# Performance work log

Measured on AMD Instinct MI355X. Metric: run time of the kernel, lower is better.

The kernel has to match this reference:

```python
import jax, jax.numpy as jnp
import numpy as np

N_CLASSES = 19


def setup_inputs() -> dict:
    key = jax.random.key(0)
    k1, k2 = jax.random.split(key)
    embedding = jax.random.normal(k1, (4, 32, 128, 128), dtype=jnp.float32)
    label = jax.random.randint(k2, (4, 512, 512), 0, N_CLASSES, dtype=jnp.int64)
    return {"embedding": embedding, "label": label}


def _discriminative_loss(embedding, label, n_classes=N_CLASSES):
    N, H, W = label.shape
    C = embedding.shape[1]
    # bilinear upsample embedding to label resolution (F.upsample mode='bilinear')
    emb = jax.image.resize(embedding, (N, C, H, W), method="bilinear")
    HW = H * W
    emb = emb.reshape(N, C, HW).transpose(0, 2, 1)          # (N, HW, C)
    lab = label.reshape(N, HW)                               # (N, HW)

    onehot = jax.nn.one_hot(lab, n_classes, dtype=emb.dtype)  # (N, HW, K)
    count = onehot.sum(1)                                    # (N, K)
    mask = (count > 0).astype(emb.dtype)                     # (N, K)

    # per-class embedding sum and (biased, /(count+1)) mean
    cls_sum = jnp.einsum("npc,npk->nkc", emb, onehot)       # (N, K, C)
    cls_mean = cls_sum / (count[:, :, None] + 1.0)           # (N, K, C)

    # intra-class: per-pixel squared distance to own-class mean, mean over C
    mean_pp = jnp.take_along_axis(cls_mean, lab[:, :, None], axis=1)  # (N, HW, C)
    d2 = jnp.mean((emb - mean_pp) ** 2, axis=-1)             # (N, HW)
    intra_per_cls = jnp.einsum("np,npk->nk", d2, onehot) / (count + 1.0)  # (N, K)
    n_fg = mask[:, 1:].sum(1)                                # (N,)
    l2_intra = (intra_per_cls[:, 1:] * mask[:, 1:]).sum(1) / n_fg  # (N,)

    # inter-class: pairwise mean squared distance between class means
    diff = cls_mean[:, :, None, :] - cls_mean[:, None, :, :]  # (N, K, K, C)
    inter = jnp.mean(diff ** 2, axis=-1)                     # (N, K, K)
    inter = inter * mask[:, None, :] * mask[:, :, None]
    l2_inter = inter[:, 1:, 1:].reshape(N, -1).sum(1) / (n_fg * n_fg)  # (N,)

    return l2_intra - l2_inter


def reference(embedding, label):
    return _discriminative_loss(embedding, label)
```

## Files before the change

kernel.cpp:

```cpp
#include <hip/hip_runtime.h>

#define NIMG 4
#define NCLS 19
#define CCH  32
#define LH   128
#define LW   128
#define HH   512
#define WW   512
#define HWQ  (LH*LW)
#define HWP  (HH*WW)

#define TR 8
#define TC 16
#define NTX (LW/TC)
#define NTY (LH/TR)
#define NTILE (NTY*NTX)
#define TCELLS (TR*TC)
#define HALO_R (TR*4+4)
#define HALO_C (TC*4+4)

#define QB 64

__device__ __forceinline__ void taps(int v, int lim, int& i0, int& i1, float& f) {
    int r = v & 3;
    int b = (v >> 2) + ((r < 2) ? -1 : 0);
    f = 0.125f + 0.25f * (float)((r + 2) & 3);
    i0 = b < 0 ? 0 : b;
    i1 = (b + 1 > lim) ? lim : (b + 1);
}

__global__ __launch_bounds__(256) void k_field(const float* __restrict__ E,
        const int* __restrict__ lab, float* __restrict__ P_sum, float* __restrict__ P_cnt) {
    int tile = blockIdx.x, n = blockIdx.y;
    int ty = tile >> 3, tx = tile & 7;
    int Y0 = ty * TR, X0 = tx * TC;
    __shared__ float A[TCELLS * NCLS];
    __shared__ float red[8 * NCLS * CCH];
    int tid = threadIdx.x;
    for (int i = tid; i < TCELLS * NCLS; i += 256) A[i] = 0.f;
    __syncthreads();

    const int* ln = lab + (size_t)n * HWP;
    int h_lo = Y0 * 4 - 2, w_lo = X0 * 4 - 2;
    for (int i = tid; i < HALO_R * HALO_C; i += 256) {
        int hr = i / HALO_C, wc = i - hr * HALO_C;
        int h = h_lo + hr, w = w_lo + wc;
        if (h < 0 || h >= HH || w < 0 || w >= WW) continue;
        int L = ln[h * WW + w];
        int y0, y1, x0, x1; float fy, fx;
        taps(h, LH - 1, y0, y1, fy);
        taps(w, LW - 1, x0, x1, fx);
        int yy[2] = {y0, y1}; float wy[2] = {1.f - fy, fy};
        int xx[2] = {x0, x1}; float wx[2] = {1.f - fx, fx};
#pragma unroll
        for (int a = 0; a < 2; a++) {
#pragma unroll
            for (int b = 0; b < 2; b++) {
                int ry = yy[a] - Y0, rx = xx[b] - X0;
                if (ry >= 0 && ry < TR && rx >= 0 && rx < TC)
                    atomicAdd(&A[(ry * TC + rx) * NCLS + L], wy[a] * wx[b]);
            }
        }
    }
    __syncthreads();

    int g = tid >> 5, c = tid & 31;
    const float* Ec = E + ((size_t)n * CCH + c) * HWQ;
    float acc[NCLS];
#pragma unroll
    for (int k = 0; k < NCLS; k++) acc[k] = 0.f;
#pragma unroll
    for (int j = 0; j < TCELLS / 8; j++) {
        int cell = g * (TCELLS / 8) + j;
        int cy = cell >> 4, cx = cell & 15;
        float e = Ec[(Y0 + cy) * LW + (X0 + cx)];
        const float* Ar = &A[cell * NCLS];
#pragma unroll
        for (int k = 0; k < NCLS; k++) acc[k] = fmaf(Ar[k], e, acc[k]);
    }
#pragma unroll
    for (int k = 0; k < NCLS; k++) red[(g * NCLS + k) * CCH + c] = acc[k];
    __syncthreads();

    float* Ps = P_sum + (size_t)(n * NTILE + tile) * (NCLS * CCH);
    for (int idx = tid; idx < NCLS * CCH; idx += 256) {
        float s = 0.f;
#pragma unroll
        for (int gg = 0; gg < 8; gg++) s += red[gg * NCLS * CCH + idx];
        Ps[idx] = s;
    }
    if (tid < NCLS) {
        float s = 0.f;
        for (int cell = 0; cell < TCELLS; cell++) s += A[cell * NCLS + tid];
        P_cnt[(size_t)(n * NTILE + tile) * NCLS + tid] = s;
    }
}

__global__ __launch_bounds__(256) void k_quad(const float* __restrict__ E,
        const int* __restrict__ lab, float* __restrict__ P_S2) {
    int n = blockIdx.y;
    int q = blockIdx.x * 256 + threadIdx.x;
    int by = q >> 7, bx = q & 127;
    __shared__ float accS2[NCLS];
    if (threadIdx.x < NCLS) accS2[threadIdx.x] = 0.f;
    __syncthreads();

    const float* En = E + (size_t)n * CCH * HWQ;
    int r0 = (by == 0) ? 0 : by - 1;
    int r2 = (by == LH - 1) ? LH - 1 : by + 1;
    int c0 = (bx == 0) ? 0 : bx - 1;
    int c2 = (bx == LW - 1) ? LW - 1 : bx + 1;
    int o0 = r0 * LW, o1 = by * LW, o2 = r2 * LW;

    float d2[16];
#pragma unroll
    for (int i = 0; i < 16; i++) d2[i] = 0.f;

    for (int c = 0; c < CCH; c++) {
        const float* Ep = En + (size_t)c * HWQ;
        float e00 = Ep[o0 + c0], e01 = Ep[o0 + bx], e02 = Ep[o0 + c2];
        float e10 = Ep[o1 + c0], e11 = Ep[o1 + bx], e12 = Ep[o1 + c2];
        float e20 = Ep[o2 + c0], e21 = Ep[o2 + bx], e22 = Ep[o2 + c2];
        float dy0 = e10 - e00, dy1 = e11 - e01, dy2 = e12 - e02;
        float dz0 = e20 - e10, dz1 = e21 - e11, dz2 = e22 - e12;
        float ry[4][3];
        ry[0][0] = fmaf(0.625f, dy0, e00); ry[0][1] = fmaf(0.625f, dy1, e01); ry[0][2] = fmaf(0.625f, dy2, e02);
        ry[1][0] = fmaf(0.875f, dy0, e00); ry[1][1] = fmaf(0.875f, dy1, e01); ry[1][2] = fmaf(0.875f, dy2, e02);
        ry[2][0] = fmaf(0.125f, dz0, e10); ry[2][1] = fmaf(0.125f, dz1, e11); ry[2][2] = fmaf(0.125f, dz2, e12);
        ry[3][0] = fmaf(0.375f, dz0, e10); ry[3][1] = fmaf(0.375f, dz1, e11); ry[3][2] = fmaf(0.375f, dz2, e12);
#pragma unroll
        for (int r = 0; r < 4; r++) {
            float da = ry[r][1] - ry[r][0], db = ry[r][2] - ry[r][1];
            float v0 = fmaf(0.625f, da, ry[r][0]);
            float v1 = fmaf(0.875f, da, ry[r][0]);
            float v2 = fmaf(0.125f, db, ry[r][1]);
            float v3 = fmaf(0.375f, db, ry[r][1]);
            d2[r * 4 + 0] = fmaf(v0, v0, d2[r * 4 + 0]);
            d2[r * 4 + 1] = fmaf(v1, v1, d2[r * 4 + 1]);
            d2[r * 4 + 2] = fmaf(v2, v2, d2[r * 4 + 2]);
            d2[r * 4 + 3] = fmaf(v3, v3, d2[r * 4 + 3]);
        }
    }
    const int* lp = lab + (size_t)n * HWP + (by * 4) * WW + bx * 4;
#pragma unroll
    for (int r = 0; r < 4; r++) {
        int4 l4 = *(const int4*)(lp + r * WW);
        atomicAdd(&accS2[l4.x], d2[r * 4 + 0]);
        atomicAdd(&accS2[l4.y], d2[r * 4 + 1]);
        atomicAdd(&accS2[l4.z], d2[r * 4 + 2]);
        atomicAdd(&accS2[l4.w], d2[r * 4 + 3]);
    }
    __syncthreads();
    if (threadIdx.x < NCLS)
        P_S2[(size_t)(n * QB + blockIdx.x) * NCLS + threadIdx.x] = accS2[threadIdx.x];
}

__global__ __launch_bounds__(384) void k_final(const float* __restrict__ P_sum,
        const float* __restrict__ P_cnt, const float* __restrict__ P_S2,
        float* __restrict__ out) {
    int n = blockIdx.x, t = threadIdx.x;
    __shared__ float csum[NCLS * 33];
    __shared__ float m[NCLS * 33];
    __shared__ float cnt[NCLS];
    __shared__ float S2[NCLS];
    __shared__ float sIntra, sNfg, sInter;

    if (t == 0) sInter = 0.f;
    if (t < NCLS) {
        float s = 0.f;
        const float* p = P_cnt + (size_t)n * NTILE * NCLS + t;
        for (int b = 0; b < NTILE; b++) s += p[b * NCLS];
        cnt[t] = s;
        float s2 = 0.f;
        const float* p2 = P_S2 + (size_t)n * QB * NCLS + t;
        for (int b = 0; b < QB; b++) s2 += p2[b * NCLS];
        S2[t] = s2;
    }
    for (int idx = t; idx < NCLS * CCH; idx += 384) {
        float s = 0.f;
        const float* p = P_sum + (size_t)n * NTILE * NCLS * CCH + idx;
        for (int b = 0; b < NTILE; b++) s += p[b * NCLS * CCH];
        csum[(idx >> 5) * 33 + (idx & 31)] = s;
    }
    __syncthreads();
    for (int idx = t; idx < NCLS * CCH; idx += 384) {
        int k = idx >> 5, c = idx & 31;
        m[k * 33 + c] = csum[k * 33 + c] / (cnt[k] + 1.f);
    }
    __syncthreads();

    float vi = 0.f, fg = 0.f;
    if (t >= 1 && t < NCLS && cnt[t] > 0.f) {
        fg = 1.f;
        float dot = 0.f, mm = 0.f;
        for (int c = 0; c < CCH; c++) {
            float mv = m[t * 33 + c];
            dot = fmaf(mv, csum[t * 33 + c], dot);
            mm = fmaf(mv, mv, mm);
        }
        vi = (S2[t] - 2.f * dot + cnt[t] * mm) * (1.f / 32.f) / (cnt[t] + 1.f);
    }
#pragma unroll
    for (int s_ = 32; s_ >= 1; s_ >>= 1) { vi += __shfl_xor(vi, s_); fg += __shfl_xor(fg, s_); }
    if (t == 0) { sIntra = vi; sNfg = fg; }

    float ve = 0.f;
    if (t < 324) {
        int j = 1 + t / 18, k = 1 + t % 18;
        if (cnt[j] > 0.f && cnt[k] > 0.f) {
            float s = 0.f;
            for (int c = 0; c < CCH; c++) {
                float d = m[j * 33 + c] - m[k * 33 + c];
                s = fmaf(d, d, s);
            }
            ve = s * (1.f / 32.f);
        }
    }
#pragma unroll
    for (int s_ = 32; s_ >= 1; s_ >>= 1) ve += __shfl_xor(ve, s_);
    if ((t & 63) == 0) atomicAdd(&sInter, ve);
    __syncthreads();
    if (t == 0) out[n] = sIntra / sNfg - sInter / (sNfg * sNfg);
}

extern "C" void kernel_launch(void* const* d_in, const int* in_sizes, int n_in,
                              void* d_out, int out_size, void* d_ws, size_t ws_size,
                              hipStream_t stream) {
    const float* E = (const float*)d_in[0];
    const int* lab = (const int*)d_in[1];
    float* out = (float*)d_out;

    float* ws = (float*)d_ws;
    float* P_sum = ws;
    float* P_cnt = P_sum + (size_t)NIMG * NTILE * NCLS * CCH;
    float* P_S2  = P_cnt + (size_t)NIMG * NTILE * NCLS;

    k_field<<<dim3(NTILE, NIMG), dim3(256), 0, stream>>>(E, lab, P_sum, P_cnt);
    k_quad <<<dim3(QB, NIMG),    dim3(256), 0, stream>>>(E, lab, P_S2);
    k_final<<<dim3(NIMG),        dim3(384), 0, stream>>>(P_sum, P_cnt, P_S2, out);
}
```

Measured before the change: 119.2 us.

## Replace per-pixel upsampled norm pass with neighbor Gram planes fused into field kernel

Instead of re-interpolating all 32 channels at each high-res pixel to get squared norms, a new kernel computes per-low-res-cell neighbor dot products (self, right, down, diagonal pairs) summed over channel chunks. The field kernel then rebuilds each pixel's squared norm from these Gram terms and its bilinear weights and accumulates it per class, which removes the separate quad kernel. The final kernel reduces the count and S2 partials in parallel. The cost is extra workspace traffic for the Gram planes (4 chunks x 5 planes), more shared-memory work per label pixel, and a changed tap-clamping scheme.

```diff
diff --git a/kernel.cpp b/kernel.cpp
--- a/kernel.cpp
+++ b/kernel.cpp
@@ -19,25 +19,86 @@
 #define HALO_R (TR*4+4)
 #define HALO_C (TC*4+4)
 
-#define QB 64
-
-__device__ __forceinline__ void taps(int v, int lim, int& i0, int& i1, float& f) {
+#define NCHUNK 4
+#define GPLANES 5
+
+__device__ __forceinline__ void taps(int v, int lim, int& i0, float& w0, float& w1) {
     int r = v & 3;
     int b = (v >> 2) + ((r < 2) ? -1 : 0);
-    f = 0.125f + 0.25f * (float)((r + 2) & 3);
-    i0 = b < 0 ? 0 : b;
-    i1 = (b + 1 > lim) ? lim : (b + 1);
+    float f = 0.125f + 0.25f * (float)((r + 2) & 3);
+    w0 = 1.f - f; w1 = f;
+    if (b < 0)           { b = 0;       w0 = 1.f; w1 = 0.f; }
+    else if (b >= lim)   { b = lim - 1; w0 = 0.f; w1 = 1.f; }
+    i0 = b;
+}
+
+__global__ __launch_bounds__(256) void k_gram(const float* __restrict__ E,
+                                              float* __restrict__ G) {
+    int n = blockIdx.y;
+    int chunk = blockIdx.x >> 6;
+    int rp    = blockIdx.x & 63;
+    int x  = threadIdx.x & 127;
+    int dy = threadIdx.x >> 7;
+    int y  = rp * 2 + dy;
+    int yp = (y < LH - 1) ? y + 1 : y;
+    int xp = (x < LW - 1) ? x + 1 : x;
+    bool lane63 = ((x & 63) == 63);
+    const float* Ep = E + ((size_t)n * CCH + chunk * 8) * HWQ;
+    float g0 = 0.f, g1 = 0.f, g2 = 0.f, g3 = 0.f, g4 = 0.f;
+#pragma unroll
+    for (int c = 0; c < 8; c++) {
+        float a  = Ep[y * LW + x];
+        float b  = Ep[yp * LW + x];
+        float ar = __shfl_down(a, 1);
+        float br = __shfl_down(b, 1);
+        if (lane63) { ar = Ep[y * LW + xp]; br = Ep[yp * LW + xp]; }
+        g0 = fmaf(a, a,  g0);
+        g1 = fmaf(a, ar, g1);
+        g2 = fmaf(a, b,  g2);
+        g3 = fmaf(a, br, g3);
+        g4 = fmaf(ar, b, g4);
+        Ep += HWQ;
+    }
+    float* Gp = G + (((size_t)n * NCHUNK + chunk) * GPLANES) * HWQ + y * LW + x;
+    Gp[0]       = g0;
+    Gp[HWQ]     = g1;
+    Gp[2 * HWQ] = g2;
+    Gp[3 * HWQ] = g3;
+    Gp[4 * HWQ] = g4;
 }
 
 __global__ __launch_bounds__(256) void k_field(const float* __restrict__ E,
-        const int* __restrict__ lab, float* __restrict__ P_sum, float* __restrict__ P_cnt) {
+        const int* __restrict__ lab, const float* __restrict__ G,
+        float* __restrict__ P_sum, float* __restrict__ P_cnt, float* __restrict__ P_S2) {
     int tile = blockIdx.x, n = blockIdx.y;
     int ty = tile >> 3, tx = tile & 7;
     int Y0 = ty * TR, X0 = tx * TC;
     __shared__ float A[TCELLS * NCLS];
     __shared__ float red[8 * NCLS * CCH];
+    __shared__ float Gt[4 * 10 * 18];
+    __shared__ float S2b[NCLS];
     int tid = threadIdx.x;
     for (int i = tid; i < TCELLS * NCLS; i += 256) A[i] = 0.f;
+    if (tid < NCLS) S2b[tid] = 0.f;
+
+    const float* Gn = G + (size_t)n * (NCHUNK * GPLANES * HWQ);
+    for (int i = tid; i < 4 * 180; i += 256) {
+        int p = i / 180, r = i % 180, gy = r / 18, gx = r % 18;
+        int yy = Y0 - 1 + gy; yy = yy < 0 ? 0 : (yy > LH - 1 ? LH - 1 : yy);
+        int xx = X0 - 1 + gx; xx = xx < 0 ? 0 : (xx > LW - 1 ? LW - 1 : xx);
+        int off = yy * LW + xx;
+        float s;
+        if (p < 3) {
+            s = Gn[(0 * GPLANES + p) * HWQ + off] + Gn[(1 * GPLANES + p) * HWQ + off]
+              + Gn[(2 * GPLANES + p) * HWQ + off] + Gn[(3 * GPLANES + p) * HWQ + off];
+        } else {
+            s = 0.f;
+#pragma unroll
+            for (int ch = 0; ch < 4; ch++)
+                s += Gn[(ch * GPLANES + 3) * HWQ + off] + Gn[(ch * GPLANES + 4) * HWQ + off];
+        }
+        Gt[i] = s;
+    }
     __syncthreads();
 
     const int* ln = lab + (size_t)n * HWP;
@@ -47,19 +108,28 @@
         int h = h_lo + hr, w = w_lo + wc;
         if (h < 0 || h >= HH || w < 0 || w >= WW) continue;
         int L = ln[h * WW + w];
-        int y0, y1, x0, x1; float fy, fx;
-        taps(h, LH - 1, y0, y1, fy);
-        taps(w, LW - 1, x0, x1, fx);
-        int yy[2] = {y0, y1}; float wy[2] = {1.f - fy, fy};
-        int xx[2] = {x0, x1}; float wx[2] = {1.f - fx, fx};
-#pragma unroll
-        for (int a = 0; a < 2; a++) {
-#pragma unroll
-            for (int b = 0; b < 2; b++) {
-                int ry = yy[a] - Y0, rx = xx[b] - X0;
-                if (ry >= 0 && ry < TR && rx >= 0 && rx < TC)
-                    atomicAdd(&A[(ry * TC + rx) * NCLS + L], wy[a] * wx[b]);
-            }
+        int y0, x0; float wy0, wy1, wx0, wx1;
+        taps(h, LH - 1, y0, wy0, wy1);
+        taps(w, LW - 1, x0, wx0, wx1);
+        int ry = y0 - Y0, rx = x0 - X0;
+        if (ry >= 0 && ry < TR) {
+            if (rx >= 0 && rx < TC)         atomicAdd(&A[(ry * TC + rx) * NCLS + L], wy0 * wx0);
+            if (rx + 1 >= 0 && rx + 1 < TC) atomicAdd(&A[(ry * TC + rx + 1) * NCLS + L], wy0 * wx1);
+        }
+        if (ry + 1 >= 0 && ry + 1 < TR) {
+            if (rx >= 0 && rx < TC)         atomicAdd(&A[((ry + 1) * TC + rx) * NCLS + L], wy1 * wx0);
+            if (rx + 1 >= 0 && rx + 1 < TC) atomicAdd(&A[((ry + 1) * TC + rx + 1) * NCLS + L], wy1 * wx1);
+        }
+        if (h >= Y0 * 4 && h < Y0 * 4 + TR * 4 && w >= X0 * 4 && w < X0 * 4 + TC * 4) {
+            int gy = y0 - (Y0 - 1), gx = x0 - (X0 - 1);
+            int g00 = gy * 18 + gx;
+            float u0 = wy0 * wy0, u1 = wy1 * wy1, u2 = wy0 * wy1;
+            float s0 = wx0 * wx0, s1 = wx1 * wx1, s2 = wx0 * wx1;
+            float d2 =
+                u0 * (s0 * Gt[g00]      + s1 * Gt[g00 + 1]  + 2.f * s2 * Gt[180 + g00])
+              + u1 * (s0 * Gt[g00 + 18] + s1 * Gt[g00 + 19] + 2.f * s2 * Gt[180 + g00 + 18])
+              + 2.f * u2 * (s0 * Gt[360 + g00] + s1 * Gt[360 + g00 + 1] + s2 * Gt[540 + g00]);
+            atomicAdd(&S2b[L], d2);
         }
     }
     __syncthreads();
@@ -93,66 +163,8 @@
         float s = 0.f;
         for (int cell = 0; cell < TCELLS; cell++) s += A[cell * NCLS + tid];
         P_cnt[(size_t)(n * NTILE + tile) * NCLS + tid] = s;
-    }
-}
-
-__global__ __launch_bounds__(256) void k_quad(const float* __restrict__ E,
-        const int* __restrict__ lab, float* __restrict__ P_S2) {
-    int n = blockIdx.y;
-    int q = blockIdx.x * 256 + threadIdx.x;
-    int by = q >> 7, bx = q & 127;
-    __shared__ float accS2[NCLS];
-    if (threadIdx.x < NCLS) accS2[threadIdx.x] = 0.f;
-    __syncthreads();
-
-    const float* En = E + (size_t)n * CCH * HWQ;
-    int r0 = (by == 0) ? 0 : by - 1;
-    int r2 = (by == LH - 1) ? LH - 1 : by + 1;
-    int c0 = (bx == 0) ? 0 : bx - 1;
-    int c2 = (bx == LW - 1) ? LW - 1 : bx + 1;
-    int o0 = r0 * LW, o1 = by * LW, o2 = r2 * LW;
-
-    float d2[16];
-#pragma unroll
-    for (int i = 0; i < 16; i++) d2[i] = 0.f;
-
-    for (int c = 0; c < CCH; c++) {
-        const float* Ep = En + (size_t)c * HWQ;
-        float e00 = Ep[o0 + c0], e01 = Ep[o0 + bx], e02 = Ep[o0 + c2];
-        float e10 = Ep[o1 + c0], e11 = Ep[o1 + bx], e12 = Ep[o1 + c2];
-        float e20 = Ep[o2 + c0], e21 = Ep[o2 + bx], e22 = Ep[o2 + c2];
-        float dy0 = e10 - e00, dy1 = e11 - e01, dy2 = e12 - e02;
-        float dz0 = e20 - e10, dz1 = e21 - e11, dz2 = e22 - e12;
-        float ry[4][3];
-        ry[0][0] = fmaf(0.625f, dy0, e00); ry[0][1] = fmaf(0.625f, dy1, e01); ry[0][2] = fmaf(0.625f, dy2, e02);
-        ry[1][0] = fmaf(0.875f, dy0, e00); ry[1][1] = fmaf(0.875f, dy1, e01); ry[1][2] = fmaf(0.875f, dy2, e02);
-        ry[2][0] = fmaf(0.125f, dz0, e10); ry[2][1] = fmaf(0.125f, dz1, e11); ry[2][2] = fmaf(0.125f, dz2, e12);
-        ry[3][0] = fmaf(0.375f, dz0, e10); ry[3][1] = fmaf(0.375f, dz1, e11); ry[3][2] = fmaf(0.375f, dz2, e12);
-#pragma unroll
-        for (int r = 0; r < 4; r++) {
-            float da = ry[r][1] - ry[r][0], db = ry[r][2] - ry[r][1];
-            float v0 = fmaf(0.625f, da, ry[r][0]);
-            float v1 = fmaf(0.875f, da, ry[r][0]);
-            float v2 = fmaf(0.125f, db, ry[r][1]);
-            float v3 = fmaf(0.375f, db, ry[r][1]);
-            d2[r * 4 + 0] = fmaf(v0, v0, d2[r * 4 + 0]);
-            d2[r * 4 + 1] = fmaf(v1, v1, d2[r * 4 + 1]);
-            d2[r * 4 + 2] = fmaf(v2, v2, d2[r * 4 + 2]);
-            d2[r * 4 + 3] = fmaf(v3, v3, d2[r * 4 + 3]);
-        }
-    }
-    const int* lp = lab + (size_t)n * HWP + (by * 4) * WW + bx * 4;
-#pragma unroll
-    for (int r = 0; r < 4; r++) {
-        int4 l4 = *(const int4*)(lp + r * WW);
-        atomicAdd(&accS2[l4.x], d2[r * 4 + 0]);
-        atomicAdd(&accS2[l4.y], d2[r * 4 + 1]);
-        atomicAdd(&accS2[l4.z], d2[r * 4 + 2]);
-        atomicAdd(&accS2[l4.w], d2[r * 4 + 3]);
-    }
-    __syncthreads();
-    if (threadIdx.x < NCLS)
-        P_S2[(size_t)(n * QB + blockIdx.x) * NCLS + threadIdx.x] = accS2[threadIdx.x];
+        P_S2[(size_t)(n * NTILE + tile) * NCLS + tid] = S2b[tid];
+    }
 }
 
 __global__ __launch_bounds__(384) void k_final(const float* __restrict__ P_sum,
@@ -163,24 +175,31 @@
     __shared__ float m[NCLS * 33];
     __shared__ float cnt[NCLS];
     __shared__ float S2[NCLS];
+    __shared__ float rk1[NCLS * 17];
+    __shared__ float rk2[NCLS * 17];
     __shared__ float sIntra, sNfg, sInter;
 
     if (t == 0) sInter = 0.f;
-    if (t < NCLS) {
-        float s = 0.f;
-        const float* p = P_cnt + (size_t)n * NTILE * NCLS + t;
-        for (int b = 0; b < NTILE; b++) s += p[b * NCLS];
-        cnt[t] = s;
-        float s2 = 0.f;
-        const float* p2 = P_S2 + (size_t)n * QB * NCLS + t;
-        for (int b = 0; b < QB; b++) s2 += p2[b * NCLS];
-        S2[t] = s2;
+    if (t < 304) {
+        int k = t >> 4, gg = t & 15;
+        const float* p1 = P_cnt + ((size_t)n * NTILE + gg * 8) * NCLS + k;
+        const float* p2 = P_S2  + ((size_t)n * NTILE + gg * 8) * NCLS + k;
+        float s1 = 0.f, s2 = 0.f;
+#pragma unroll
+        for (int j = 0; j < 8; j++) { s1 += p1[j * NCLS]; s2 += p2[j * NCLS]; }
+        rk1[k * 17 + gg] = s1; rk2[k * 17 + gg] = s2;
     }
     for (int idx = t; idx < NCLS * CCH; idx += 384) {
         float s = 0.f;
         const float* p = P_sum + (size_t)n * NTILE * NCLS * CCH + idx;
         for (int b = 0; b < NTILE; b++) s += p[b * NCLS * CCH];
         csum[(idx >> 5) * 33 + (idx & 31)] = s;
+    }
+    __syncthreads();
+    if (t < NCLS) {
+        float s1 = 0.f, s2 = 0.f;
+        for (int gg = 0; gg < 16; gg++) { s1 += rk1[t * 17 + gg]; s2 += rk2[t * 17 + gg]; }
+        cnt[t] = s1; S2[t] = s2;
     }
     __syncthreads();
     for (int idx = t; idx < NCLS * CCH; idx += 384) {
@@ -234,8 +253,9 @@
     float* P_sum = ws;
     float* P_cnt = P_sum + (size_t)NIMG * NTILE * NCLS * CCH;
     float* P_S2  = P_cnt + (size_t)NIMG * NTILE * NCLS;
-
-    k_field<<<dim3(NTILE, NIMG), dim3(256), 0, stream>>>(E, lab, P_sum, P_cnt);
-    k_quad <<<dim3(QB, NIMG),    dim3(256), 0, stream>>>(E, lab, P_S2);
+    float* G     = P_S2  + (size_t)NIMG * NTILE * NCLS;
+
+    k_gram <<<dim3(256, NIMG),   dim3(256), 0, stream>>>(E, G);
+    k_field<<<dim3(NTILE, NIMG), dim3(256), 0, stream>>>(E, lab, G, P_sum, P_cnt, P_S2);
     k_final<<<dim3(NIMG),        dim3(384), 0, stream>>>(P_sum, P_cnt, P_S2, out);
 }
```

After: 116.0 us. 1.03x faster.
